# Performance work log

Hardware: AMD Instinct MI355X
Metric: run time of the kernel (lower is better)

Reference implementation:

```python
import jax, jax.numpy as jnp
import numpy as np

N_NODES = 100_000
N_EDGES = 3_200_000
IN_DIM = 32
HID = 64
LN_EPS = 1e-5


def setup_inputs() -> dict:
    key = jax.random.key(0)
    ks = jax.random.split(key, 6)

    def lin_w(k, fan_in, fan_out):
        # torch Linear default init ~ U(-1/sqrt(fan_in), 1/sqrt(fan_in)); randn/sqrt(fan_in) is fine for a numeric baseline
        return (jax.random.normal(k, (fan_in, fan_out), jnp.float32) / np.sqrt(fan_in)).astype(jnp.float32)

    return {
        "x_edge": jax.random.normal(ks[0], (N_EDGES, IN_DIM), jnp.float32),
        "edge_index": jax.random.randint(ks[1], (N_EDGES, 2), 0, N_NODES, jnp.int64),
        "num_nodes": N_NODES,
        "W1": lin_w(ks[2], IN_DIM, HID), "b1": jnp.zeros((HID,), jnp.float32),
        "W2": lin_w(ks[3], HID, HID),   "b2": jnp.zeros((HID,), jnp.float32),
        "W3": lin_w(ks[4], HID, HID),   "b3": jnp.zeros((HID,), jnp.float32),
        "W4": lin_w(ks[5], HID, HID),   "b4": jnp.zeros((HID,), jnp.float32),
        "gamma": jnp.ones((HID,), jnp.float32),
        "beta": jnp.zeros((HID,), jnp.float32),
    }


def reference(x_edge, edge_index, num_nodes, W1, b1, W2, b2, W3, b3, W4, b4, gamma, beta):
    # 4-layer edge MLP: Linear+ReLU x3, Linear, then LayerNorm over feature dim
    h = jax.nn.relu(x_edge @ W1 + b1)
    h = jax.nn.relu(h @ W2 + b2)
    h = jax.nn.relu(h @ W3 + b3)
    h = h @ W4 + b4  # [E, HID]
    mu = jnp.mean(h, axis=-1, keepdims=True)
    var = jnp.mean(jnp.square(h - mu), axis=-1, keepdims=True)
    x_edge1 = gamma * (h - mu) * jax.lax.rsqrt(var + LN_EPS) + beta  # [E, HID]

    # double scatter_add into node buffer: add edge feature to both endpoints
    x_node = (jax.ops.segment_sum(x_edge1, edge_index[:, 0], num_segments=num_nodes)
              + jax.ops.segment_sum(x_edge1, edge_index[:, 1], num_segments=num_nodes))  # [N, HID]
    return x_node, x_edge1
```

## Files before the change

kernel.cpp:

```cpp
#include <hip/hip_runtime.h>
#include <hip/hip_bf16.h>

#define IN_DIM 32
#define HID 64
#define LN_EPS 1e-5f
#define BSH 3
#define BCAP 1024
#define CSH 10

typedef unsigned short ush;
typedef unsigned int u32;
typedef unsigned long long u64;
typedef __attribute__((ext_vector_type(8))) short bf16x8;
typedef __attribute__((ext_vector_type(4))) float f32x4;
typedef __attribute__((ext_vector_type(4))) unsigned int u32x4;

static __device__ __forceinline__ float b2f(u32 u) {
    union { u32 i; float f; } v; v.i = u << 16; return v.f;
}
static __device__ __forceinline__ ush f2b(float f) {
    union { float f; u32 i; } v; v.f = f;
    u32 x = v.i;
    return (ush)((x + 0x7fffu + ((x >> 16) & 1u)) >> 16);
}
static __device__ __forceinline__ ush f2bh(float f) {
    union { __hip_bfloat16 h; ush u; } v;
    v.h = __float2bfloat16(f);
    return v.u;
}

__global__ __launch_bounds__(256) void zero_i32(int* __restrict__ p, int n) {
    const int i = blockIdx.x * 256 + threadIdx.x;
    if (i < n) p[i] = 0;
}

__global__ __launch_bounds__(256) void zero16(uint4* __restrict__ p, int n16) {
    const int i = blockIdx.x * 256 + threadIdx.x;
    if (i < n16) p[i] = make_uint4(0u, 0u, 0u, 0u);
}

static __device__ __forceinline__ bool sniff_idx64(const int* idx) {
    int zc = 0;
    #pragma unroll
    for (int t = 0; t < 8; ++t) zc += (idx[2 * t + 1] == 0) ? 1 : 0;
    return zc >= 7;
}

__global__ __launch_bounds__(256) void pack_and_init(
    const float* __restrict__ W1, const float* __restrict__ W2,
    const float* __restrict__ W3, const float* __restrict__ W4,
    ush* __restrict__ pack, int* __restrict__ bcur, int NB)
{
    const int i = blockIdx.x * 256 + threadIdx.x;
    if (i < NB) bcur[i] = i << CSH;
    if (i >= 14336) return;
    const float* W; int base;
    if (i < 2048)       { W = W1; base = 0; }
    else if (i < 6144)  { W = W2; base = 2048; }
    else if (i < 10240) { W = W3; base = 6144; }
    else                { W = W4; base = 10240; }
    const int j = i - base;
    const int e = j & 7, l = (j >> 3) & 63, f = j >> 9;
    const int ct = f & 3, kc = f >> 2;
    const int k = kc * 32 + ((l >> 4) << 3) + e;
    const int col = ct * 16 + (l & 15);
    pack[i] = f2b(W[k * HID + col]);
}


__global__ __launch_bounds__(256) void bucket_count(
    const int* __restrict__ idx, int* __restrict__ bcnt, int E, int N)
{
    const bool idx64 = sniff_idx64(idx);
    const int e = blockIdx.x * 256 + threadIdx.x;
    if (e >= E) return;
    int na, nb;
    if (idx64) { const int4 p = ((const int4*)idx)[e]; na = p.x; nb = p.z; }
    else       { const int2 p = ((const int2*)idx)[e]; na = p.x; nb = p.y; }
    na = min(max(na, 0), N - 1);
    nb = min(max(nb, 0), N - 1);
    atomicAdd(&bcnt[na >> BSH], 1);
    atomicAdd(&bcnt[nb >> BSH], 1);
}

__global__ __launch_bounds__(1024) void scan_excl2(
    int* __restrict__ a, int* __restrict__ b, int n)
{
    __shared__ int lds[1024];
    const int t = threadIdx.x;
    const int L = (n + 1023) >> 10;
    const int lo = t * L, hi = min(n, lo + L);
    int s = 0;
    for (int i = lo; i < hi; ++i) s += a[i];
    lds[t] = s;
    __syncthreads();
    #pragma unroll
    for (int d = 1; d < 1024; d <<= 1) {
        const int v = (t >= d) ? lds[t - d] : 0;
        __syncthreads();
        lds[t] += v;
        __syncthreads();
    }
    int run = lds[t] - s;
    for (int i = lo; i < hi; ++i) {
        const int c = a[i];
        a[i] = run; b[i] = run;
        run += c;
    }
}

__global__ __launch_bounds__(256) void append_pairs(
    const int* __restrict__ idx, int* __restrict__ bcur,
    u32* __restrict__ buf, int E, int N)
{
    const bool idx64 = sniff_idx64(idx);
    const int e = blockIdx.x * 256 + threadIdx.x;
    if (e >= E) return;
    int na, nb;
    if (idx64) { const int4 p = ((const int4*)idx)[e]; na = p.x; nb = p.z; }
    else       { const int2 p = ((const int2*)idx)[e]; na = p.x; nb = p.y; }
    na = min(max(na, 0), N - 1);
    nb = min(max(nb, 0), N - 1);
    const int pa = atomicAdd(&bcur[na >> BSH], 1);
    buf[pa] = ((u32)(na & ((1 << BSH) - 1)) << 29) | (u32)e;
    const int pb = atomicAdd(&bcur[nb >> BSH], 1);
    buf[pb] = ((u32)(nb & ((1 << BSH) - 1)) << 29) | (u32)e;
}

template <int FIXED>
__global__ __launch_bounds__(256) void bucket_sort(
    const int* __restrict__ bstart, const int* __restrict__ bend,
    u32* __restrict__ buf, int* __restrict__ nstart, int NB, int N)
{
    __shared__ u32 stg[4][BCAP];
    const int tid = threadIdx.x, wave = tid >> 6, lane = tid & 63;
    const int b = blockIdx.x * 4 + wave;
    if (b >= NB) return;
    const int s = FIXED ? (b << CSH) : bstart[b];
    const int e = bend[b], len = e - s;
    const int node0 = b << BSH;

    if (len > BCAP) {
        if (lane < 8 && node0 + lane < N) nstart[node0 + lane] = -1;
        return;
    }

    for (int i = lane; i < len; i += 64) stg[wave][i] = buf[s + i];

    int c[8] = {0, 0, 0, 0, 0, 0, 0, 0};
    for (int i = lane; i < len; i += 64) ++c[stg[wave][i] >> 29];
    #pragma unroll
    for (int k = 0; k < 8; ++k) {
        int v = c[k];
        #pragma unroll
        for (int m = 1; m < 64; m <<= 1) v += __shfl_xor(v, m, 64);
        c[k] = v;
    }
    u32 run[8];
    {
        u32 acc = 0;
        #pragma unroll
        for (int k = 0; k < 8; ++k) { run[k] = acc; acc += (u32)c[k]; }
    }
    if (lane < 8 && node0 + lane < N) nstart[node0 + lane] = s + (int)run[lane];

    for (int i0 = 0; i0 < len; i0 += 64) {
        const int i = i0 + lane;
        const bool val = i < len;
        const u32 ent = val ? stg[wave][i] : 0u;
        const int k = (int)(ent >> 29);
        u32 pos = 0;
        #pragma unroll
        for (int kk = 0; kk < 8; ++kk) {
            const u64 m = __ballot(val && (k == kk));
            if (val && k == kk)
                pos = run[kk] + (u32)__popcll(m & ((1ull << lane) - 1ull));
            run[kk] += (u32)__popcll(m);
        }
        if (val) buf[s + pos] = ent;
    }
}

template <int FIXED>
__global__ __launch_bounds__(256) void node_gather_bf(
    const int* __restrict__ nstart,
    const int* __restrict__ bstart, const int* __restrict__ bend,
    const u32* __restrict__ buf,
    const u32* __restrict__ ebf,
    float* __restrict__ out_node, int N)
{
    const int w = (blockIdx.x * 256 + threadIdx.x) >> 6;
    const int lane = threadIdx.x & 63;
    if (w >= N) return;
    const int half = lane >> 5, j = lane & 31;
    const int b = w >> BSH;

    float ax = 0.f, ay = 0.f;
    const int s0 = nstart[w];
    if (s0 >= 0) {
        const bool lastInB = ((w & ((1 << BSH) - 1)) == ((1 << BSH) - 1)) || (w == N - 1);
        const int e0 = lastInB ? bend[b] : nstart[w + 1];
        int i = s0;
        for (; i + 16 <= e0; i += 16) {
            u32 ent[8];
            #pragma unroll
            for (int u = 0; u < 8; ++u) ent[u] = buf[i + half * 8 + u];
            u32 rv[8];
            #pragma unroll
            for (int u = 0; u < 8; ++u)
                rv[u] = ebf[(size_t)(ent[u] & 0x1FFFFFFFu) * 32 + j];
            #pragma unroll
            for (int u = 0; u < 8; ++u) {
                ax += b2f(rv[u] & 0xffffu);
                ay += b2f(rv[u] >> 16);
            }
        }
        for (int ii = i + half; ii < e0; ii += 2) {
            const u32 v = ebf[(size_t)(buf[ii] & 0x1FFFFFFFu) * 32 + j];
            ax += b2f(v & 0xffffu);
            ay += b2f(v >> 16);
        }
    } else {
        if (half == 0) {
            const u32 key = (u32)(w & ((1 << BSH) - 1)) << 29;
            const int s = FIXED ? (b << CSH) : bstart[b];
            const int e = bend[b];
            for (int i = s; i < e; ++i) {
                const u32 en = buf[i];
                if ((en & 0xE0000000u) == key) {
                    const u32 v = ebf[(size_t)(en & 0x1FFFFFFFu) * 32 + j];
                    ax += b2f(v & 0xffffu);
                    ay += b2f(v >> 16);
                }
            }
        }
    }
    ax += __shfl_xor(ax, 32, 64);
    ay += __shfl_xor(ay, 32, 64);
    if (half == 0) {
        float2 o; o.x = ax; o.y = ay;
        *(float2*)(out_node + (size_t)w * HID + 2 * j) = o;
    }
}

__global__ __launch_bounds__(256) void node_gather(
    const int* __restrict__ nstart,
    const int* __restrict__ bstart, const int* __restrict__ bend,
    const u32* __restrict__ buf,
    const float* __restrict__ edge_feat,
    float* __restrict__ out_node, int N)
{
    const int w = (blockIdx.x * 256 + threadIdx.x) >> 6;
    const int lane = threadIdx.x & 63;
    if (w >= N) return;
    const int b = w >> BSH;

    float acc = 0.f;
    const int s0 = nstart[w];
    if (s0 >= 0) {
        const bool lastInB = ((w & ((1 << BSH) - 1)) == ((1 << BSH) - 1)) || (w == N - 1);
        const int e0 = lastInB ? bend[b] : nstart[w + 1];
        int i = s0;
        for (; i + 16 <= e0; i += 16) {
            u32 ent[16];
            #pragma unroll
            for (int u = 0; u < 16; ++u) ent[u] = buf[i + u];
            float v[16];
            #pragma unroll
            for (int u = 0; u < 16; ++u)
                v[u] = edge_feat[(size_t)(ent[u] & 0x1FFFFFFFu) * HID + lane];
            #pragma unroll
            for (int u = 0; u < 16; ++u) acc += v[u];
        }
        for (; i < e0; ++i)
            acc += edge_feat[(size_t)(buf[i] & 0x1FFFFFFFu) * HID + lane];
    } else {
        const u32 key = (u32)(w & ((1 << BSH) - 1)) << 29;
        const int s = bstart[b], e = bend[b];
        for (int i = s; i < e; ++i) {
            const u32 en = buf[i];
            if ((en & 0xE0000000u) == key)
                acc += edge_feat[(size_t)(en & 0x1FFFFFFFu) * HID + lane];
        }
    }
    out_node[(size_t)w * HID + lane] = acc;
}

__global__ __launch_bounds__(256) void pack_weights(
    const float* __restrict__ W1, const float* __restrict__ W2,
    const float* __restrict__ W3, const float* __restrict__ W4,
    ush* __restrict__ pack)
{
    const int i = blockIdx.x * 256 + threadIdx.x;
    if (i >= 14336) return;
    const float* W; int base;
    if (i < 2048)       { W = W1; base = 0; }
    else if (i < 6144)  { W = W2; base = 2048; }
    else if (i < 10240) { W = W3; base = 6144; }
    else                { W = W4; base = 10240; }
    const int j = i - base;
    const int e = j & 7, l = (j >> 3) & 63, f = j >> 9;
    const int ct = f & 3, kc = f >> 2;
    const int k = kc * 32 + ((l >> 4) << 3) + e;
    const int col = ct * 16 + (l & 15);
    pack[i] = f2b(W[k * HID + col]);
}

template <int APPEND>
__global__ __launch_bounds__(512, 6) void mlp_ln_mfma(
    const float* __restrict__ x,
    const ush* __restrict__ packW,
    const float* __restrict__ b1, const float* __restrict__ b2,
    const float* __restrict__ b3, const float* __restrict__ b4,
    const float* __restrict__ gamma, const float* __restrict__ beta,
    float* __restrict__ out_edge,
    u32* __restrict__ ebf,
    int write_bf,
    const int* __restrict__ idx,
    int* __restrict__ bcur,
    u32* __restrict__ buf,
    int E, int N)
{
    __shared__ float sB[6 * HID];
    __shared__ __align__(16) ush sW[14336];
    __shared__ __align__(16) ush hbuf[8][16 * 72];

    const int tid = threadIdx.x;
    const int wave = tid >> 6, lane = tid & 63;

    if (APPEND) {
        const int e = blockIdx.x * 128 + tid;
        if (tid < 128 && e < E) {
            const bool idx64 = sniff_idx64(idx);
            int na, nb;
            if (idx64) { const int4 p = ((const int4*)idx)[e]; na = p.x; nb = p.z; }
            else       { const int2 p = ((const int2*)idx)[e]; na = p.x; nb = p.y; }
            na = min(max(na, 0), N - 1);
            nb = min(max(nb, 0), N - 1);
            const int pa = atomicAdd(&bcur[na >> BSH], 1);
            buf[pa] = ((u32)(na & ((1 << BSH) - 1)) << 29) | (u32)e;
            const int pb = atomicAdd(&bcur[nb >> BSH], 1);
            buf[pb] = ((u32)(nb & ((1 << BSH) - 1)) << 29) | (u32)e;
        }
    }

    {
        const uint4* src = (const uint4*)packW;
        uint4* dst = (uint4*)sW;
        #pragma unroll
        for (int i = 0; i < 4; ++i) {
            const int o = tid + i * 512;
            if (o < 1792) dst[o] = src[o];
        }
    }
    if (tid < HID) {
        sB[tid]           = b1[tid];
        sB[HID + tid]     = b2[tid];
        sB[2 * HID + tid] = b3[tid];
        sB[3 * HID + tid] = b4[tid];
        sB[4 * HID + tid] = gamma[tid];
        sB[5 * HID + tid] = beta[tid];
    }
    __syncthreads();

    const bf16x8* wfrag = (const bf16x8*)sW;

    ush* hb = &hbuf[wave][0];
    const int l15 = lane & 15, lg = lane >> 4;

    const int rowBase = blockIdx.x * 128 + wave * 16;

    const int rr = min(rowBase + l15, E - 1);
    const f32x4* xp = (const f32x4*)(x + (size_t)rr * IN_DIM + lg * 8);
    const f32x4 xa = __builtin_nontemporal_load(xp);
    const f32x4 xb = __builtin_nontemporal_load(xp + 1);
    bf16x8 aL1;
    aL1[0] = (short)f2bh(xa[0]); aL1[1] = (short)f2bh(xa[1]);
    aL1[2] = (short)f2bh(xa[2]); aL1[3] = (short)f2bh(xa[3]);
    aL1[4] = (short)f2bh(xb[0]); aL1[5] = (short)f2bh(xb[1]);
    aL1[6] = (short)f2bh(xb[2]); aL1[7] = (short)f2bh(xb[3]);

    f32x4 acc[4];

    #pragma unroll
    for (int ct = 0; ct < 4; ++ct) {
        const float bv = sB[0 * HID + ct * 16 + l15];
        f32x4 c = {bv, bv, bv, bv};
        const bf16x8 wf = wfrag[0 + ct * 64 + lane];
        c = __builtin_amdgcn_mfma_f32_16x16x32_bf16(aL1, wf, c, 0, 0, 0);
        acc[ct] = c;
    }

    #pragma unroll
    for (int ct = 0; ct < 4; ++ct)
        #pragma unroll
        for (int r = 0; r < 4; ++r) {
            float v = acc[ct][r]; v = v > 0.f ? v : 0.f;
            hb[(lg * 4 + r) * 72 + ct * 16 + l15] = f2bh(v);
        }

    #define LAYER(WBASE, BIDX, RELU_) do {                                  \
        const bf16x8 a0 = *(const bf16x8*)&hb[l15 * 72 + 0 * 32 + lg * 8];  \
        const bf16x8 a1 = *(const bf16x8*)&hb[l15 * 72 + 1 * 32 + lg * 8];  \
        _Pragma("unroll")                                                   \
        for (int ct = 0; ct < 4; ++ct) {                                    \
            const float bv = sB[(BIDX) * HID + ct * 16 + l15];              \
            f32x4 c = {bv, bv, bv, bv};                                     \
            const bf16x8 wlo = wfrag[(WBASE) + ct * 64 + lane];             \
            const bf16x8 whi = wfrag[(WBASE) + (4 + ct) * 64 + lane];       \
            c = __builtin_amdgcn_mfma_f32_16x16x32_bf16(a0, wlo, c, 0, 0, 0); \
            c = __builtin_amdgcn_mfma_f32_16x16x32_bf16(a1, whi, c, 0, 0, 0); \
            acc[ct] = c;                                                    \
        }                                                                   \
        if (RELU_) {                                                        \
            _Pragma("unroll")                                               \
            for (int ct = 0; ct < 4; ++ct)                                  \
                _Pragma("unroll")                                           \
                for (int r = 0; r < 4; ++r) {                               \
                    float v = acc[ct][r]; v = v > 0.f ? v : 0.f;            \
                    hb[(lg * 4 + r) * 72 + ct * 16 + l15] = f2bh(v);        \
                }                                                           \
        }                                                                   \
    } while (0)

    LAYER(256, 1, 1);
    LAYER(768, 2, 1);
    LAYER(1280, 3, 0);
    #undef LAYER

    float s1[4], s2[4];
    #pragma unroll
    for (int r = 0; r < 4; ++r) {
        float a = acc[0][r] + acc[1][r] + acc[2][r] + acc[3][r];
        float q = acc[0][r] * acc[0][r] + acc[1][r] * acc[1][r]
                + acc[2][r] * acc[2][r] + acc[3][r] * acc[3][r];
        #pragma unroll
        for (int m = 1; m < 16; m <<= 1) {
            a += __shfl_xor(a, m, 64);
            q += __shfl_xor(q, m, 64);
        }
        s1[r] = a; s2[r] = q;
    }

    #pragma unroll
    for (int r = 0; r < 4; ++r) {
        const float mu = s1[r] * (1.0f / HID);
        const float varr = fmaxf(s2[r] * (1.0f / HID) - mu * mu, 0.f);
        const float inv = rsqrtf(varr + LN_EPS);
        const int row = rowBase + lg * 4 + r;
        float* op = out_edge + (size_t)row * HID;
        #pragma unroll
        for (int ct = 0; ct < 4; ++ct) {
            const float g = sB[4 * HID + ct * 16 + l15];
            const float bt = sB[5 * HID + ct * 16 + l15];
            const float val = g * (acc[ct][r] - mu) * inv + bt;
            if (row < E) op[ct * 16 + l15] = val;
            hb[(lg * 4 + r) * 72 + ct * 16 + l15] = f2bh(val);
        }
    }

    if (write_bf) {
        const int rloc = lane >> 2, ch = lane & 3;
        const int row = rowBase + rloc;
        if (row < E) {
            const u32x4* bsrc = (const u32x4*)&hb[rloc * 72 + ch * 16];
            u32x4* bdst = (u32x4*)(ebf + (size_t)row * 32 + ch * 8);
            bdst[0] = bsrc[0];
            bdst[1] = bsrc[1];
        }
    }
}

__global__ __launch_bounds__(256) void mlp_ln_scatter_fb(
    const float* __restrict__ x, const int* __restrict__ idx,
    const float* __restrict__ W1, const float* __restrict__ b1,
    const float* __restrict__ W2, const float* __restrict__ b2,
    const float* __restrict__ W3, const float* __restrict__ b3,
    const float* __restrict__ W4, const float* __restrict__ b4,
    const float* __restrict__ gamma, const float* __restrict__ beta,
    float* __restrict__ out_edge, float* __restrict__ node_acc, int E, int N)
{
    __shared__ float sW1[IN_DIM * HID];
    __shared__ float sW2[HID * HID];
    __shared__ float sW3[HID * HID];
    __shared__ float sW4[HID * HID];
    __shared__ float sB[6 * HID];
    const int tid = threadIdx.x;
    {
        const float4* W1v = (const float4*)W1;
        float4* s1 = (float4*)sW1;
        for (int i = tid; i < IN_DIM * HID / 4; i += 256) s1[i] = W1v[i];
        const float4* W2v = (const float4*)W2;
        const float4* W3v = (const float4*)W3;
        const float4* W4v = (const float4*)W4;
        float4* s2 = (float4*)sW2; float4* s3 = (float4*)sW3; float4* s4 = (float4*)sW4;
        for (int i = tid; i < HID * HID / 4; i += 256) { s2[i] = W2v[i]; s3[i] = W3v[i]; s4[i] = W4v[i]; }
        if (tid < HID) {
            sB[tid] = b1[tid]; sB[HID + tid] = b2[tid]; sB[2 * HID + tid] = b3[tid];
            sB[3 * HID + tid] = b4[tid]; sB[4 * HID + tid] = gamma[tid]; sB[5 * HID + tid] = beta[tid];
        }
    }
    __syncthreads();
    const int e = blockIdx.x * 256 + tid;
    if (e >= E) return;
    float h0[IN_DIM];
    {
        const float4* xv = (const float4*)(x + (size_t)e * IN_DIM);
        #pragma unroll
        for (int c = 0; c < 8; ++c) {
            const float4 v = xv[c];
            h0[c * 4 + 0] = v.x; h0[c * 4 + 1] = v.y; h0[c * 4 + 2] = v.z; h0[c * 4 + 3] = v.w;
        }
    }
    float a[HID], h[HID];
    #pragma unroll
    for (int j = 0; j < HID; ++j) a[j] = sB[j];
    #pragma unroll
    for (int k = 0; k < IN_DIM; ++k) {
        const float hk = h0[k];
        #pragma unroll
        for (int j = 0; j < HID; ++j) a[j] = fmaf(hk, sW1[k * HID + j], a[j]);
    }
    #pragma unroll
    for (int j = 0; j < HID; ++j) h[j] = a[j] > 0.f ? a[j] : 0.f;
    #pragma unroll
    for (int j = 0; j < HID; ++j) a[j] = sB[HID + j];
    #pragma unroll
    for (int k = 0; k < HID; ++k) {
        const float hk = h[k];
        #pragma unroll
        for (int j = 0; j < HID; ++j) a[j] = fmaf(hk, sW2[k * HID + j], a[j]);
    }
    #pragma unroll
    for (int j = 0; j < HID; ++j) h[j] = a[j] > 0.f ? a[j] : 0.f;
    #pragma unroll
    for (int j = 0; j < HID; ++j) a[j] = sB[2 * HID + j];
    #pragma unroll
    for (int k = 0; k < HID; ++k) {
        const float hk = h[k];
        #pragma unroll
        for (int j = 0; j < HID; ++j) a[j] = fmaf(hk, sW3[k * HID + j], a[j]);
    }
    #pragma unroll
    for (int j = 0; j < HID; ++j) h[j] = a[j] > 0.f ? a[j] : 0.f;
    #pragma unroll
    for (int j = 0; j < HID; ++j) a[j] = sB[3 * HID + j];
    #pragma unroll
    for (int k = 0; k < HID; ++k) {
        const float hk = h[k];
        #pragma unroll
        for (int j = 0; j < HID; ++j) a[j] = fmaf(hk, sW4[k * HID + j], a[j]);
    }
    float s = 0.f;
    #pragma unroll
    for (int j = 0; j < HID; ++j) s += a[j];
    const float mu = s * (1.0f / HID);
    float s2 = 0.f;
    #pragma unroll
    for (int j = 0; j < HID; ++j) { const float d = a[j] - mu; s2 += d * d; }
    const float inv = rsqrtf(s2 * (1.0f / HID) + LN_EPS);
    #pragma unroll
    for (int j = 0; j < HID; ++j)
        a[j] = sB[4 * HID + j] * ((a[j] - mu) * inv) + sB[5 * HID + j];
    {
        float4* oe = (float4*)(out_edge + (size_t)e * HID);
        #pragma unroll
        for (int c = 0; c < 16; ++c)
            oe[c] = make_float4(a[c * 4], a[c * 4 + 1], a[c * 4 + 2], a[c * 4 + 3]);
    }
    const bool idx64 = sniff_idx64(idx);
    int na, nb;
    if (idx64) { na = idx[4 * (size_t)e]; nb = idx[4 * (size_t)e + 2]; }
    else       { na = idx[2 * (size_t)e]; nb = idx[2 * (size_t)e + 1]; }
    na = min(max(na, 0), N - 1);
    nb = min(max(nb, 0), N - 1);
    float* pa = node_acc + (size_t)na * HID;
    float* pb = node_acc + (size_t)nb * HID;
    #pragma unroll
    for (int j = 0; j < HID; ++j) {
        unsafeAtomicAdd(pa + j, a[j]);
        unsafeAtomicAdd(pb + j, a[j]);
    }
}

extern "C" void kernel_launch(void* const* d_in, const int* in_sizes, int n_in,
                              void* d_out, int out_size, void* d_ws, size_t ws_size,
                              hipStream_t stream) {
    const float* x     = (const float*)d_in[0];
    const int*   idx   = (const int*)d_in[1];
    const float* W1    = (const float*)d_in[3];
    const float* b1    = (const float*)d_in[4];
    const float* W2    = (const float*)d_in[5];
    const float* b2    = (const float*)d_in[6];
    const float* W3    = (const float*)d_in[7];
    const float* b3    = (const float*)d_in[8];
    const float* W4    = (const float*)d_in[9];
    const float* b4    = (const float*)d_in[10];
    const float* gamma = (const float*)d_in[11];
    const float* beta  = (const float*)d_in[12];

    const int E = in_sizes[0] / IN_DIM;
    const int N = out_size / HID - E;
    const int NB = (N + (1 << BSH) - 1) >> BSH;

    float* out_node = (float*)d_out;
    float* out_edge = out_node + (size_t)N * HID;

    const size_t bcurOffF   = 32768;
    const size_t nstartOffF = bcurOffF + (((size_t)NB * 4 + 255) & ~255ull);
    const size_t bufOffF    = nstartOffF + (((size_t)N * 4 + 255) & ~255ull);
    const size_t ebfOffF    = (bufOffF + ((size_t)NB << CSH) * 4 + 255) & ~255ull;
    const size_t need_fixed = ebfOffF + (size_t)E * 32 * sizeof(u32);

    const size_t bstartOff = 32768;
    const size_t bcurOff   = bstartOff + (((size_t)NB * 4 + 255) & ~255ull);
    const size_t nstartOff = bcurOff + (((size_t)NB * 4 + 255) & ~255ull);
    const size_t bufOff    = nstartOff + (((size_t)N * 4 + 255) & ~255ull);
    const size_t ebfOff    = (bufOff + (size_t)2 * E * sizeof(u32) + 255) & ~255ull;
    const size_t need_base = bufOff + (size_t)2 * E * sizeof(u32);
    const size_t need_bf   = ebfOff + (size_t)E * 32 * sizeof(u32);

    if (ws_size >= need_fixed) {
        ush* pack   = (ush*)d_ws;
        int* bcur   = (int*)((char*)d_ws + bcurOffF);
        int* nstart = (int*)((char*)d_ws + nstartOffF);
        u32* buf    = (u32*)((char*)d_ws + bufOffF);
        u32* ebf    = (u32*)((char*)d_ws + ebfOffF);

        pack_and_init<<<(14336 + 255) / 256, 256, 0, stream>>>(
            W1, W2, W3, W4, pack, bcur, NB);
        mlp_ln_mfma<1><<<(E + 127) / 128, 512, 0, stream>>>(
            x, pack, b1, b2, b3, b4, gamma, beta, out_edge, ebf, 1,
            idx, bcur, buf, E, N);
        bucket_sort<1><<<(NB + 3) / 4, 256, 0, stream>>>(
            nullptr, bcur, buf, nstart, NB, N);
        node_gather_bf<1><<<(N * 64 + 255) / 256, 256, 0, stream>>>(
            nstart, nullptr, bcur, buf, ebf, out_node, N);
    } else if (ws_size >= need_base) {
        ush* pack   = (ush*)d_ws;
        int* bstart = (int*)((char*)d_ws + bstartOff);
        int* bcur   = (int*)((char*)d_ws + bcurOff);
        int* nstart = (int*)((char*)d_ws + nstartOff);
        u32* buf    = (u32*)((char*)d_ws + bufOff);
        u32* ebf    = (u32*)((char*)d_ws + ebfOff);
        const int use_bf = (ws_size >= need_bf) ? 1 : 0;

        pack_weights<<<(14336 + 255) / 256, 256, 0, stream>>>(W1, W2, W3, W4, pack);
        zero_i32<<<(NB + 255) / 256, 256, 0, stream>>>(bstart, NB);
        bucket_count<<<(E + 255) / 256, 256, 0, stream>>>(idx, bstart, E, N);
        scan_excl2<<<1, 1024, 0, stream>>>(bstart, bcur, NB);
        append_pairs<<<(E + 255) / 256, 256, 0, stream>>>(idx, bcur, buf, E, N);
        bucket_sort<0><<<(NB + 3) / 4, 256, 0, stream>>>(bstart, bcur, buf, nstart, NB, N);
        mlp_ln_mfma<0><<<(E + 127) / 128, 512, 0, stream>>>(
            x, pack, b1, b2, b3, b4, gamma, beta, out_edge, ebf, use_bf,
            nullptr, nullptr, nullptr, E, N);
        if (use_bf) {
            node_gather_bf<0><<<(N * 64 + 255) / 256, 256, 0, stream>>>(
                nstart, bstart, bcur, buf, ebf, out_node, N);
        } else {
            node_gather<<<(N * 64 + 255) / 256, 256, 0, stream>>>(
                nstart, bstart, bcur, buf, out_edge, out_node, N);
        }
    } else {
        const int n16 = (int)(((size_t)N * HID * sizeof(float)) / 16);
        zero16<<<(n16 + 255) / 256, 256, 0, stream>>>((uint4*)out_node, n16);
        mlp_ln_scatter_fb<<<(E + 255) / 256, 256, 0, stream>>>(
            x, idx, W1, b1, W2, b2, W3, b3, W4, b4, gamma, beta,
            out_edge, out_node, E, N);
    }
}
```

Measured before the change: 723.6 us.

## Swap MFMA operands so each lane holds one edge row's features

Weights become the A operand and activations the B operand of each MFMA. The accumulator then holds four consecutive feature columns of a single edge row per lane instead of one column across four rows. This allows packed 8-byte bf16 stores into the LDS staging buffer, vectorized bias/gamma/beta loads, and a LayerNorm reduction of only two cross-lane shuffles per row. Output fp32 and bf16 edge rows are written directly from registers with 16-byte and 8-byte stores, removing the LDS round trip for the bf16 copy. The cost is that each lane writes a strided row segment instead of the old coalesced per-column pattern, and correctness depends on the weight fragments being valid in the swapped operand role.

```diff
diff --git a/kernel.cpp b/kernel.cpp
--- a/kernel.cpp
+++ b/kernel.cpp
@@ -23,10 +23,10 @@
     u32 x = v.i;
     return (ush)((x + 0x7fffu + ((x >> 16) & 1u)) >> 16);
 }
-static __device__ __forceinline__ ush f2bh(float f) {
+static __device__ __forceinline__ u32 f2bh(float f) {
     union { __hip_bfloat16 h; ush u; } v;
     v.h = __float2bfloat16(f);
-    return v.u;
+    return (u32)v.u;
 }
 
 __global__ __launch_bounds__(256) void zero_i32(int* __restrict__ p, int n) {
@@ -383,43 +383,49 @@
     f32x4 acc[4];
 
     #pragma unroll
-    for (int ct = 0; ct < 4; ++ct) {
-        const float bv = sB[0 * HID + ct * 16 + l15];
-        f32x4 c = {bv, bv, bv, bv};
-        const bf16x8 wf = wfrag[0 + ct * 64 + lane];
-        c = __builtin_amdgcn_mfma_f32_16x16x32_bf16(aL1, wf, c, 0, 0, 0);
-        acc[ct] = c;
-    }
-
-    #pragma unroll
-    for (int ct = 0; ct < 4; ++ct)
-        #pragma unroll
-        for (int r = 0; r < 4; ++r) {
-            float v = acc[ct][r]; v = v > 0.f ? v : 0.f;
-            hb[(lg * 4 + r) * 72 + ct * 16 + l15] = f2bh(v);
-        }
+    for (int mt = 0; mt < 4; ++mt) {
+        f32x4 c = *(const f32x4*)&sB[0 * HID + mt * 16 + lg * 4];
+        const bf16x8 wf = wfrag[mt * 64 + lane];
+        c = __builtin_amdgcn_mfma_f32_16x16x32_bf16(wf, aL1, c, 0, 0, 0);
+        acc[mt] = c;
+    }
+
+    #pragma unroll
+    for (int mt = 0; mt < 4; ++mt) {
+        const float v0 = fmaxf(acc[mt][0], 0.f);
+        const float v1 = fmaxf(acc[mt][1], 0.f);
+        const float v2 = fmaxf(acc[mt][2], 0.f);
+        const float v3 = fmaxf(acc[mt][3], 0.f);
+        uint2 pk;
+        pk.x = f2bh(v0) | (f2bh(v1) << 16);
+        pk.y = f2bh(v2) | (f2bh(v3) << 16);
+        *(uint2*)&hb[l15 * 72 + mt * 16 + lg * 4] = pk;
+    }
 
     #define LAYER(WBASE, BIDX, RELU_) do {                                  \
-        const bf16x8 a0 = *(const bf16x8*)&hb[l15 * 72 + 0 * 32 + lg * 8];  \
-        const bf16x8 a1 = *(const bf16x8*)&hb[l15 * 72 + 1 * 32 + lg * 8];  \
+        const bf16x8 a0 = *(const bf16x8*)&hb[l15 * 72 + 0 + lg * 8];       \
+        const bf16x8 a1 = *(const bf16x8*)&hb[l15 * 72 + 32 + lg * 8];      \
         _Pragma("unroll")                                                   \
-        for (int ct = 0; ct < 4; ++ct) {                                    \
-            const float bv = sB[(BIDX) * HID + ct * 16 + l15];              \
-            f32x4 c = {bv, bv, bv, bv};                                     \
-            const bf16x8 wlo = wfrag[(WBASE) + ct * 64 + lane];             \
-            const bf16x8 whi = wfrag[(WBASE) + (4 + ct) * 64 + lane];       \
-            c = __builtin_amdgcn_mfma_f32_16x16x32_bf16(a0, wlo, c, 0, 0, 0); \
-            c = __builtin_amdgcn_mfma_f32_16x16x32_bf16(a1, whi, c, 0, 0, 0); \
-            acc[ct] = c;                                                    \
+        for (int mt = 0; mt < 4; ++mt) {                                    \
+            f32x4 c = *(const f32x4*)&sB[(BIDX) * HID + mt * 16 + lg * 4];  \
+            const bf16x8 wlo = wfrag[(WBASE) + mt * 64 + lane];             \
+            const bf16x8 whi = wfrag[(WBASE) + (4 + mt) * 64 + lane];       \
+            c = __builtin_amdgcn_mfma_f32_16x16x32_bf16(wlo, a0, c, 0, 0, 0); \
+            c = __builtin_amdgcn_mfma_f32_16x16x32_bf16(whi, a1, c, 0, 0, 0); \
+            acc[mt] = c;                                                    \
         }                                                                   \
         if (RELU_) {                                                        \
             _Pragma("unroll")                                               \
-            for (int ct = 0; ct < 4; ++ct)                                  \
-                _Pragma("unroll")                                           \
-                for (int r = 0; r < 4; ++r) {                               \
-                    float v = acc[ct][r]; v = v > 0.f ? v : 0.f;            \
-                    hb[(lg * 4 + r) * 72 + ct * 16 + l15] = f2bh(v);        \
-                }                                                           \
+            for (int mt = 0; mt < 4; ++mt) {                                \
+                const float v0 = fmaxf(acc[mt][0], 0.f);                    \
+                const float v1 = fmaxf(acc[mt][1], 0.f);                    \
+                const float v2 = fmaxf(acc[mt][2], 0.f);                    \
+                const float v3 = fmaxf(acc[mt][3], 0.f);                    \
+                uint2 pk;                                                   \
+                pk.x = f2bh(v0) | (f2bh(v1) << 16);                         \
+                pk.y = f2bh(v2) | (f2bh(v3) << 16);                         \
+                *(uint2*)&hb[l15 * 72 + mt * 16 + lg * 4] = pk;             \
+            }                                                               \
         }                                                                   \
     } while (0)
 
@@ -428,45 +434,39 @@
     LAYER(1280, 3, 0);
     #undef LAYER
 
-    float s1[4], s2[4];
-    #pragma unroll
-    for (int r = 0; r < 4; ++r) {
-        float a = acc[0][r] + acc[1][r] + acc[2][r] + acc[3][r];
-        float q = acc[0][r] * acc[0][r] + acc[1][r] * acc[1][r]
-                + acc[2][r] * acc[2][r] + acc[3][r] * acc[3][r];
-        #pragma unroll
-        for (int m = 1; m < 16; m <<= 1) {
-            a += __shfl_xor(a, m, 64);
-            q += __shfl_xor(q, m, 64);
-        }
-        s1[r] = a; s2[r] = q;
-    }
-
-    #pragma unroll
-    for (int r = 0; r < 4; ++r) {
-        const float mu = s1[r] * (1.0f / HID);
-        const float varr = fmaxf(s2[r] * (1.0f / HID) - mu * mu, 0.f);
-        const float inv = rsqrtf(varr + LN_EPS);
-        const int row = rowBase + lg * 4 + r;
+    float s = 0.f, q = 0.f;
+    #pragma unroll
+    for (int mt = 0; mt < 4; ++mt)
+        #pragma unroll
+        for (int r = 0; r < 4; ++r) {
+            const float v = acc[mt][r];
+            s += v; q += v * v;
+        }
+    s += __shfl_xor(s, 16, 64); q += __shfl_xor(q, 16, 64);
+    s += __shfl_xor(s, 32, 64); q += __shfl_xor(q, 32, 64);
+    const float mu = s * (1.0f / HID);
+    const float varr = fmaxf(q * (1.0f / HID) - mu * mu, 0.f);
+    const float inv = rsqrtf(varr + LN_EPS);
+
+    const int row = rowBase + l15;
+    if (row < E) {
         float* op = out_edge + (size_t)row * HID;
-        #pragma unroll
-        for (int ct = 0; ct < 4; ++ct) {
-            const float g = sB[4 * HID + ct * 16 + l15];
-            const float bt = sB[5 * HID + ct * 16 + l15];
-            const float val = g * (acc[ct][r] - mu) * inv + bt;
-            if (row < E) op[ct * 16 + l15] = val;
-            hb[(lg * 4 + r) * 72 + ct * 16 + l15] = f2bh(val);
-        }
-    }
-
-    if (write_bf) {
-        const int rloc = lane >> 2, ch = lane & 3;
-        const int row = rowBase + rloc;
-        if (row < E) {
-            const u32x4* bsrc = (const u32x4*)&hb[rloc * 72 + ch * 16];
-            u32x4* bdst = (u32x4*)(ebf + (size_t)row * 32 + ch * 8);
-            bdst[0] = bsrc[0];
-            bdst[1] = bsrc[1];
+        u32* ep = ebf + (size_t)row * 32;
+        #pragma unroll
+        for (int mt = 0; mt < 4; ++mt) {
+            const f32x4 g4 = *(const f32x4*)&sB[4 * HID + mt * 16 + lg * 4];
+            const f32x4 bt4 = *(const f32x4*)&sB[5 * HID + mt * 16 + lg * 4];
+            f32x4 o;
+            #pragma unroll
+            for (int r = 0; r < 4; ++r)
+                o[r] = g4[r] * (acc[mt][r] - mu) * inv + bt4[r];
+            *(f32x4*)(op + mt * 16 + lg * 4) = o;
+            if (write_bf) {
+                uint2 pk;
+                pk.x = f2bh(o[0]) | (f2bh(o[1]) << 16);
+                pk.y = f2bh(o[2]) | (f2bh(o[3]) << 16);
+                *(uint2*)(ep + mt * 8 + lg * 2) = pk;
+            }
         }
     }
 }
```

After: 823.6 us. 13.8% more time.

## Fuse bucket sort and node gather into one kernel using LDS-sorted entries

Applied to the files above, without the earlier changes.

In the fixed-capacity workspace path, the per-bucket counting sort and the per-node gather are combined into a single 512-thread kernel. Each block sorts its bucket's entries in shared memory and then gathers edge features per node directly. This removes the write-back of sorted entries, the nstart array and a kernel launch. In exchange, the sort runs on one wave while the others wait, and bucket length is clamped to the shared capacity with no overflow fallback.

```diff
diff --git a/kernel.cpp b/kernel.cpp
--- a/kernel.cpp
+++ b/kernel.cpp
@@ -23,10 +23,10 @@
     u32 x = v.i;
     return (ush)((x + 0x7fffu + ((x >> 16) & 1u)) >> 16);
 }
-static __device__ __forceinline__ ush f2bh(float f) {
+static __device__ __forceinline__ u32 f2bh(float f) {
     union { __hip_bfloat16 h; ush u; } v;
     v.h = __float2bfloat16(f);
-    return v.u;
+    return (u32)v.u;
 }
 
 __global__ __launch_bounds__(256) void zero_i32(int* __restrict__ p, int n) {
@@ -127,7 +127,6 @@
     buf[pb] = ((u32)(nb & ((1 << BSH) - 1)) << 29) | (u32)e;
 }
 
-template <int FIXED>
 __global__ __launch_bounds__(256) void bucket_sort(
     const int* __restrict__ bstart, const int* __restrict__ bend,
     u32* __restrict__ buf, int* __restrict__ nstart, int NB, int N)
@@ -136,7 +135,7 @@
     const int tid = threadIdx.x, wave = tid >> 6, lane = tid & 63;
     const int b = blockIdx.x * 4 + wave;
     if (b >= NB) return;
-    const int s = FIXED ? (b << CSH) : bstart[b];
+    const int s = bstart[b];
     const int e = bend[b], len = e - s;
     const int node0 = b << BSH;
 
@@ -181,7 +180,98 @@
     }
 }
 
-template <int FIXED>
+__global__ __launch_bounds__(512) void sort_gather_bf(
+    const int* __restrict__ bend,
+    const u32* __restrict__ buf,
+    const u32* __restrict__ ebf,
+    float* __restrict__ out_node, int NB, int N)
+{
+    __shared__ u32 stg[BCAP];
+    __shared__ u32 srt[BCAP];
+    __shared__ int snst[9];
+
+    const int tid = threadIdx.x, wave = tid >> 6, lane = tid & 63;
+    const int b = blockIdx.x;
+    const int s = b << CSH;
+    const int len = min(bend[b] - s, BCAP);
+    const int node0 = b << BSH;
+
+    for (int i = tid; i < len; i += 512) stg[i] = buf[s + i];
+    __syncthreads();
+
+    if (wave == 0) {
+        int c[8] = {0, 0, 0, 0, 0, 0, 0, 0};
+        for (int i = lane; i < len; i += 64) ++c[stg[i] >> 29];
+        #pragma unroll
+        for (int k = 0; k < 8; ++k) {
+            int v = c[k];
+            #pragma unroll
+            for (int m = 1; m < 64; m <<= 1) v += __shfl_xor(v, m, 64);
+            c[k] = v;
+        }
+        u32 run[8];
+        {
+            u32 acc = 0;
+            #pragma unroll
+            for (int k = 0; k < 8; ++k) { run[k] = acc; acc += (u32)c[k]; }
+        }
+        if (lane == 0) {
+            #pragma unroll
+            for (int k = 0; k < 8; ++k) snst[k] = (int)run[k];
+            snst[8] = len;
+        }
+        for (int i0 = 0; i0 < len; i0 += 64) {
+            const int i = i0 + lane;
+            const bool val = i < len;
+            const u32 ent = val ? stg[i] : 0u;
+            const int k = (int)(ent >> 29);
+            u32 pos = 0;
+            #pragma unroll
+            for (int kk = 0; kk < 8; ++kk) {
+                const u64 m = __ballot(val && (k == kk));
+                if (val && k == kk)
+                    pos = run[kk] + (u32)__popcll(m & ((1ull << lane) - 1ull));
+                run[kk] += (u32)__popcll(m);
+            }
+            if (val) srt[pos] = ent;
+        }
+    }
+    __syncthreads();
+
+    const int w = node0 + wave;
+    if (w >= N) return;
+    const int half = lane >> 5, j = lane & 31;
+    const int s0 = snst[wave], e0 = snst[wave + 1];
+
+    float ax = 0.f, ay = 0.f;
+    int i = s0;
+    for (; i + 16 <= e0; i += 16) {
+        u32 ent[8];
+        #pragma unroll
+        for (int u = 0; u < 8; ++u) ent[u] = srt[i + half * 8 + u];
+        u32 rv[8];
+        #pragma unroll
+        for (int u = 0; u < 8; ++u)
+            rv[u] = ebf[(size_t)(ent[u] & 0x1FFFFFFFu) * 32 + j];
+        #pragma unroll
+        for (int u = 0; u < 8; ++u) {
+            ax += b2f(rv[u] & 0xffffu);
+            ay += b2f(rv[u] >> 16);
+        }
+    }
+    for (int ii = i + half; ii < e0; ii += 2) {
+        const u32 v = ebf[(size_t)(srt[ii] & 0x1FFFFFFFu) * 32 + j];
+        ax += b2f(v & 0xffffu);
+        ay += b2f(v >> 16);
+    }
+    ax += __shfl_xor(ax, 32, 64);
+    ay += __shfl_xor(ay, 32, 64);
+    if (half == 0) {
+        float2 o; o.x = ax; o.y = ay;
+        *(float2*)(out_node + (size_t)w * HID + 2 * j) = o;
+    }
+}
+
 __global__ __launch_bounds__(256) void node_gather_bf(
     const int* __restrict__ nstart,
     const int* __restrict__ bstart, const int* __restrict__ bend,
@@ -223,8 +313,7 @@
     } else {
         if (half == 0) {
             const u32 key = (u32)(w & ((1 << BSH) - 1)) << 29;
-            const int s = FIXED ? (b << CSH) : bstart[b];
-            const int e = bend[b];
+            const int s = bstart[b], e = bend[b];
             for (int i = s; i < e; ++i) {
                 const u32 en = buf[i];
                 if ((en & 0xE0000000u) == key) {
@@ -396,7 +485,7 @@
         #pragma unroll
         for (int r = 0; r < 4; ++r) {
             float v = acc[ct][r]; v = v > 0.f ? v : 0.f;
-            hb[(lg * 4 + r) * 72 + ct * 16 + l15] = f2bh(v);
+            hb[(lg * 4 + r) * 72 + ct * 16 + l15] = (ush)f2bh(v);
         }
 
     #define LAYER(WBASE, BIDX, RELU_) do {                                  \
@@ -418,7 +507,7 @@
                 _Pragma("unroll")                                           \
                 for (int r = 0; r < 4; ++r) {                               \
                     float v = acc[ct][r]; v = v > 0.f ? v : 0.f;            \
-                    hb[(lg * 4 + r) * 72 + ct * 16 + l15] = f2bh(v);        \
+                    hb[(lg * 4 + r) * 72 + ct * 16 + l15] = (ush)f2bh(v);   \
                 }                                                           \
         }                                                                   \
     } while (0)
@@ -455,7 +544,7 @@
             const float bt = sB[5 * HID + ct * 16 + l15];
             const float val = g * (acc[ct][r] - mu) * inv + bt;
             if (row < E) op[ct * 16 + l15] = val;
-            hb[(lg * 4 + r) * 72 + ct * 16 + l15] = f2bh(val);
+            hb[(lg * 4 + r) * 72 + ct * 16 + l15] = (ush)f2bh(val);
         }
     }
 
@@ -623,7 +712,6 @@
     if (ws_size >= need_fixed) {
         ush* pack   = (ush*)d_ws;
         int* bcur   = (int*)((char*)d_ws + bcurOffF);
-        int* nstart = (int*)((char*)d_ws + nstartOffF);
         u32* buf    = (u32*)((char*)d_ws + bufOffF);
         u32* ebf    = (u32*)((char*)d_ws + ebfOffF);
 
@@ -632,10 +720,7 @@
         mlp_ln_mfma<1><<<(E + 127) / 128, 512, 0, stream>>>(
             x, pack, b1, b2, b3, b4, gamma, beta, out_edge, ebf, 1,
             idx, bcur, buf, E, N);
-        bucket_sort<1><<<(NB + 3) / 4, 256, 0, stream>>>(
-            nullptr, bcur, buf, nstart, NB, N);
-        node_gather_bf<1><<<(N * 64 + 255) / 256, 256, 0, stream>>>(
-            nstart, nullptr, bcur, buf, ebf, out_node, N);
+        sort_gather_bf<<<NB, 512, 0, stream>>>(bcur, buf, ebf, out_node, NB, N);
     } else if (ws_size >= need_base) {
         ush* pack   = (ush*)d_ws;
         int* bstart = (int*)((char*)d_ws + bstartOff);
@@ -650,12 +735,12 @@
         bucket_count<<<(E + 255) / 256, 256, 0, stream>>>(idx, bstart, E, N);
         scan_excl2<<<1, 1024, 0, stream>>>(bstart, bcur, NB);
         append_pairs<<<(E + 255) / 256, 256, 0, stream>>>(idx, bcur, buf, E, N);
-        bucket_sort<0><<<(NB + 3) / 4, 256, 0, stream>>>(bstart, bcur, buf, nstart, NB, N);
+        bucket_sort<<<(NB + 3) / 4, 256, 0, stream>>>(bstart, bcur, buf, nstart, NB, N);
         mlp_ln_mfma<0><<<(E + 127) / 128, 512, 0, stream>>>(
             x, pack, b1, b2, b3, b4, gamma, beta, out_edge, ebf, use_bf,
             nullptr, nullptr, nullptr, E, N);
         if (use_bf) {
-            node_gather_bf<0><<<(N * 64 + 255) / 256, 256, 0, stream>>>(
+            node_gather_bf<<<(N * 64 + 255) / 256, 256, 0, stream>>>(
                 nstart, bstart, bcur, buf, ebf, out_node, N);
         } else {
             node_gather<<<(N * 64 + 255) / 256, 256, 0, stream>>>(
```

New measurement: 705.0 us. 2.6% less time.
